# Kernel optimization log

Hardware: AMD Instinct MI355X
Metric: run time of the kernel (lower is better)

The kernel has to match this reference:

```python
import jax, jax.numpy as jnp
import numpy as np

DIM = 1536; FFN = 8960; NH = 12; HD = DIM // NH
B = 1; Fg, Hg, Wg = 8, 20, 20; L = Fg * Hg * Wg; L2 = 512
EPS = 1e-6; MAXLEN = 1024


def _rope_tables():
    # Wan rope_params: per-axis inverse-frequency tables, concatenated [t|h|w]
    c = HD // 2; c0 = c - 2 * (c // 3); c1 = c // 3
    def ang(dp):
        inv = 1.0 / (10000.0 ** (np.arange(0, dp, 2, dtype=np.float64) / dp))
        return np.outer(np.arange(MAXLEN, dtype=np.float64), inv)
    a = np.concatenate([ang(2 * c0), ang(2 * c1), ang(2 * c1)], axis=1)  # [1024, c]
    return np.cos(a).astype(np.float32), np.sin(a).astype(np.float32)


def setup_inputs() -> dict:
    key = jax.random.key(0)
    ks = jax.random.split(key, 32); it = iter(range(32))
    def rnd(shape, scale=0.02):
        return jax.random.normal(ks[next(it)], shape, dtype=jnp.float32) * scale
    cos, sin = _rope_tables()
    inp = {
        'x': rnd((B, L, DIM), 1.0),
        'e': rnd((B, 6, DIM), 1.0),
        'context': rnd((B, L2, DIM), 1.0),
        'freqs_cos': jnp.asarray(cos), 'freqs_sin': jnp.asarray(sin),
        'modulation': rnd((1, 6, DIM), DIM ** -0.5),
    }
    for p in ['sa', 'ca']:
        for nm in ['q', 'k', 'v', 'o']:
            inp[p + '_' + nm + 'w'] = rnd((DIM, DIM))
            inp[p + '_' + nm + 'b'] = jnp.zeros((DIM,), jnp.float32)
        inp[p + '_nq'] = jnp.ones((DIM,), jnp.float32)
        inp[p + '_nk'] = jnp.ones((DIM,), jnp.float32)
    inp['n3_w'] = jnp.ones((DIM,), jnp.float32); inp['n3_b'] = jnp.zeros((DIM,), jnp.float32)
    inp['ffn_w1'] = rnd((DIM, FFN)); inp['ffn_b1'] = jnp.zeros((FFN,), jnp.float32)
    inp['ffn_w2'] = rnd((FFN, DIM)); inp['ffn_b2'] = jnp.zeros((DIM,), jnp.float32)
    inp['grid_f'] = Fg; inp['grid_h'] = Hg; inp['grid_w'] = Wg
    return inp


def _layer_norm(x, w=None, b=None):
    mu = x.mean(-1, keepdims=True)
    var = jnp.mean((x - mu) ** 2, -1, keepdims=True)
    y = (x - mu) * jax.lax.rsqrt(var + EPS)
    return y * w + b if w is not None else y


def _rms(x, w):
    return x * jax.lax.rsqrt(jnp.mean(x * x, -1, keepdims=True) + EPS) * w


def _rope(xq, cos, sin, f, h, w):
    # xq: [B, L, n, d]; complex rotation per (t,h,w) axis with split freq dims
    b, s, n, d = xq.shape
    c = d // 2; c0 = c - 2 * (c // 3); c1 = c // 3
    def grid(tab):
        t = jnp.broadcast_to(tab[:f, None, None, :c0], (f, h, w, c0))
        hh = jnp.broadcast_to(tab[None, :h, None, c0:c0 + c1], (f, h, w, c1))
        ww = jnp.broadcast_to(tab[None, None, :w, c0 + c1:c0 + 2 * c1], (f, h, w, c1))
        return jnp.concatenate([t, hh, ww], -1).reshape(f * h * w, c)
    gc = grid(cos)[None, :, None, :]  # [1, L, 1, c]
    gs = grid(sin)[None, :, None, :]
    xr = xq.reshape(b, s, n, c, 2)
    xre, xim = xr[..., 0], xr[..., 1]
    return jnp.stack([xre * gc - xim * gs, xre * gs + xim * gc], -1).reshape(b, s, n, d)


def _attn(q, k, v):
    scores = jnp.einsum('bqnd,bknd->bnqk', q, k) * (q.shape[-1] ** -0.5)
    p = jax.nn.softmax(scores, -1)
    return jnp.einsum('bnqk,bknd->bqnd', p, v)


def reference(x, e, context, freqs_cos, freqs_sin, modulation,
              sa_qw, sa_qb, sa_kw, sa_kb, sa_vw, sa_vb, sa_ow, sa_ob, sa_nq, sa_nk,
              ca_qw, ca_qb, ca_kw, ca_kb, ca_vw, ca_vb, ca_ow, ca_ob, ca_nq, ca_nk,
              n3_w, n3_b, ffn_w1, ffn_b1, ffn_w2, ffn_b2,
              grid_f, grid_h, grid_w):
    b, s, _ = x.shape; n, d = NH, HD
    em = modulation + e  # [B, 6, C]
    e0, e1, e2, e3, e4, e5 = (em[:, i:i + 1] for i in range(6))
    # self-attention with adaLN modulation
    xs = _layer_norm(x) * (1 + e1) + e0
    q = _rms(xs @ sa_qw + sa_qb, sa_nq).reshape(b, s, n, d)
    k = _rms(xs @ sa_kw + sa_kb, sa_nk).reshape(b, s, n, d)
    v = (xs @ sa_vw + sa_vb).reshape(b, s, n, d)
    q = _rope(q, freqs_cos, freqs_sin, grid_f, grid_h, grid_w)
    k = _rope(k, freqs_cos, freqs_sin, grid_f, grid_h, grid_w)
    y = _attn(q, k, v).reshape(b, s, -1) @ sa_ow + sa_ob
    x = x + y * e2
    # cross-attention on norm3(x)
    xc = _layer_norm(x, n3_w, n3_b)
    s2 = context.shape[1]
    cq = _rms(xc @ ca_qw + ca_qb, ca_nq).reshape(b, s, n, d)
    ck = _rms(context @ ca_kw + ca_kb, ca_nk).reshape(b, s2, n, d)
    cv = (context @ ca_vw + ca_vb).reshape(b, s2, n, d)
    x = x + (_attn(cq, ck, cv).reshape(b, s, -1) @ ca_ow + ca_ob)
    # FFN with adaLN modulation
    xf = _layer_norm(x) * (1 + e4) + e3
    y = jax.nn.gelu(xf @ ffn_w1 + ffn_b1, approximate=True) @ ffn_w2 + ffn_b2
    return x + y * e5
```

## Files before the change

kernel.cpp:

```cpp
#include <hip/hip_runtime.h>

#define DIM 1536
#define NH 12
#define HD 128
#define LQ 3200
#define LKV 512
#define FFN 8960

typedef __attribute__((ext_vector_type(8))) short bf16x8;
typedef __attribute__((ext_vector_type(4))) float f32x4;
typedef __attribute__((ext_vector_type(4))) unsigned short u16x4;

__device__ inline unsigned short f2b(float f){
  union { float f; unsigned u; } x; x.f = f;
  unsigned r = (x.u + 0x7FFFu + ((x.u >> 16) & 1u)) >> 16;
  return (unsigned short)r;
}
__device__ inline float b2f(unsigned short u){
  union { unsigned u; float f; } x; x.u = ((unsigned)u) << 16; return x.f;
}
__device__ inline unsigned pack2(float a, float b){
  return (unsigned)f2b(a) | ((unsigned)f2b(b) << 16);
}
__device__ inline f32x4 mfma16(bf16x8 a, bf16x8 b, f32x4 c){
  return __builtin_amdgcn_mfma_f32_16x16x32_bf16(a, b, c, 0, 0, 0);
}
__device__ inline void gload_lds16(const unsigned short* g, unsigned short* l){
  __builtin_amdgcn_global_load_lds((const __attribute__((address_space(1))) unsigned int*)g,
                                   (__attribute__((address_space(3))) unsigned int*)l, 16, 0, 0);
}
__device__ inline int xcd_swizzle(int orig, int nwg){
  int q = nwg >> 3, r = nwg & 7;
  int xcd = orig & 7, off = orig >> 3;
  return (xcd < r ? xcd*(q+1) : r*(q+1) + (xcd-r)*q) + off;
}
__device__ inline float gelu_f(float vv){
  float u = 0.79788456080286535588f*(vv + 0.044715f*vv*vv*vv);
  u = fminf(fmaxf(u, -20.f), 20.f);
  float e2u = __expf(2.f*u);
  float th = (e2u - 1.f)/(e2u + 1.f);
  return 0.5f*vv*(1.f+th);
}


__global__ void add_vec(const float* __restrict__ a, const float* __restrict__ b,
                        float* __restrict__ o, int n){
  int i = blockIdx.x*256 + threadIdx.x;
  if (i < n) o[i] = a[i] + b[i];
}

__global__ void convert_bf16(const float* __restrict__ a, unsigned short* __restrict__ o, int n){
  int i = blockIdx.x*256 + threadIdx.x;
  if (i < n) o[i] = f2b(a[i]);
}

__global__ void concat3(const float* __restrict__ a, const float* __restrict__ b,
                        const float* __restrict__ c, float* __restrict__ o, int n){
  int i = blockIdx.x*256 + threadIdx.x;
  if (i < n) o[i] = a[i];
  else if (i < 2*n) o[i] = b[i - n];
  else if (i < 3*n) o[i] = c[i - 2*n];
}

__global__ void transpose_conv(const float* __restrict__ src, unsigned short* __restrict__ dst,
                               int K, int N){
  __shared__ float tile[32][33];
  int n0 = blockIdx.x*32, k0 = blockIdx.y*32;
  int tx = threadIdx.x, ty = threadIdx.y;
  #pragma unroll
  for (int i = 0; i < 4; i++)
    tile[ty + 8*i][tx] = src[(size_t)(k0 + ty + 8*i)*N + n0 + tx];
  __syncthreads();
  #pragma unroll
  for (int i = 0; i < 4; i++)
    dst[(size_t)(n0 + ty + 8*i)*K + k0 + tx] = f2b(tile[tx][ty + 8*i]);
}

__global__ __launch_bounds__(256) void ln_mod_kernel(const float* __restrict__ x,
    const float* __restrict__ mulv, const float* __restrict__ addv, int one_plus,
    unsigned short* __restrict__ out){
  int row = blockIdx.x;
  const float* xr = x + (size_t)row * DIM;
  int tid = threadIdx.x;
  float v[6]; float s = 0.f, ss = 0.f;
  #pragma unroll
  for (int i = 0; i < 6; i++){ v[i] = xr[tid + i*256]; s += v[i]; ss += v[i]*v[i]; }
  #pragma unroll
  for (int m = 1; m < 64; m <<= 1){ s += __shfl_xor(s, m, 64); ss += __shfl_xor(ss, m, 64); }
  __shared__ float bs[4], bss[4];
  int w = tid >> 6;
  if ((tid & 63) == 0){ bs[w] = s; bss[w] = ss; }
  __syncthreads();
  s = bs[0]+bs[1]+bs[2]+bs[3]; ss = bss[0]+bss[1]+bss[2]+bss[3];
  float mu  = s * (1.f/DIM);
  float var = ss * (1.f/DIM) - mu*mu;
  float inv = rsqrtf(var + 1e-6f);
  unsigned short* orow = out + (size_t)row*DIM;
  #pragma unroll
  for (int i = 0; i < 6; i++){
    int c = tid + i*256;
    float g = one_plus ? (1.f + mulv[c]) : mulv[c];
    orow[c] = f2b((v[i]-mu)*inv*g + addv[c]);
  }
}

__global__ __launch_bounds__(256) void reduce_ln_kernel(const float* P0, const float* P1,
    const float* bias, const float* resid, const float* svec, float* out_x,
    const float* mulv, const float* addv, int one_plus, unsigned short* out_ln){
  int row = blockIdx.x;
  size_t base = (size_t)row * DIM;
  int tid = threadIdx.x;
  float v[6]; float s = 0.f, ss = 0.f;
  #pragma unroll
  for (int i = 0; i < 6; i++){
    int c = tid + i*256;
    float sv = svec ? svec[c] : 1.f;
    float y = resid[base + c] + (P0[base + c] + P1[base + c] + bias[c])*sv;
    out_x[base + c] = y;
    v[i] = y; s += y; ss += y*y;
  }
  #pragma unroll
  for (int m = 1; m < 64; m <<= 1){ s += __shfl_xor(s, m, 64); ss += __shfl_xor(ss, m, 64); }
  __shared__ float bs[4], bss[4];
  int w = tid >> 6;
  if ((tid & 63) == 0){ bs[w] = s; bss[w] = ss; }
  __syncthreads();
  s = bs[0]+bs[1]+bs[2]+bs[3]; ss = bss[0]+bss[1]+bss[2]+bss[3];
  float mu  = s * (1.f/DIM);
  float var = ss * (1.f/DIM) - mu*mu;
  float inv = rsqrtf(var + 1e-6f);
  unsigned short* orow = out_ln + base;
  #pragma unroll
  for (int i = 0; i < 6; i++){
    int c = tid + i*256;
    float g = one_plus ? (1.f + mulv[c]) : mulv[c];
    orow[c] = f2b((v[i]-mu)*inv*g + addv[c]);
  }
}

__global__ __launch_bounds__(256) void reduce_rms_kernel(const float* __restrict__ P0,
    const float* __restrict__ P1, const float* __restrict__ bias,
    const float* __restrict__ nw, unsigned short* __restrict__ out){
  int row = blockIdx.x;
  size_t base = (size_t)row * DIM;
  int tid = threadIdx.x;
  float v[6]; float ss = 0.f;
  #pragma unroll
  for (int i = 0; i < 6; i++){
    int c = tid + i*256;
    float y = P0[base + c] + P1[base + c] + bias[c];
    v[i] = y; ss += y*y;
  }
  #pragma unroll
  for (int m = 1; m < 64; m <<= 1) ss += __shfl_xor(ss, m, 64);
  __shared__ float bss[4];
  if ((tid & 63) == 0) bss[tid >> 6] = ss;
  __syncthreads();
  ss = bss[0]+bss[1]+bss[2]+bss[3];
  float inv = rsqrtf(ss*(1.f/DIM) + 1e-6f);
  #pragma unroll
  for (int i = 0; i < 6; i++){
    int c = tid + i*256;
    out[base + c] = f2b(v[i]*inv*nw[c]);
  }
}

__global__ __launch_bounds__(256) void rms_rope_qk(unsigned short* __restrict__ buf,
    const float* __restrict__ nwq, const float* __restrict__ nwk,
    const float* __restrict__ ct, const float* __restrict__ st){
  int row = blockIdx.x;
  int sl = blockIdx.y;
  const float* nw = sl ? nwk : nwq;
  unsigned short* xr = buf + (size_t)row*(3*DIM) + sl*DIM;
  int tid = threadIdx.x;
  float ss = 0.f; float v[6];
  #pragma unroll
  for (int i = 0; i < 6; i++){ v[i] = b2f(xr[tid + i*256]); ss += v[i]*v[i]; }
  #pragma unroll
  for (int m = 1; m < 64; m <<= 1) ss += __shfl_xor(ss, m, 64);
  __shared__ float bss[4];
  if ((tid & 63) == 0) bss[tid >> 6] = ss;
  __syncthreads();
  ss = bss[0]+bss[1]+bss[2]+bss[3];
  float inv = rsqrtf(ss*(1.f/DIM) + 1e-6f);
  int f = row/400, hp = (row/20)%20, wp = row%20;
  for (int p = tid; p < 768; p += 256){
    int hh = p >> 6, j = p & 63;
    int pos = (j < 22) ? f : ((j < 43) ? hp : wp);
    float c_ = ct[pos*64 + j], s_ = st[pos*64 + j];
    int base = hh*HD + 2*j;
    float xre = b2f(xr[base])   * inv * nw[base];
    float xim = b2f(xr[base+1]) * inv * nw[base+1];
    xr[base]   = f2b(xre*c_ - xim*s_);
    xr[base+1] = f2b(xre*s_ + xim*c_);
  }
}

__global__ __launch_bounds__(256) void rms_rope_b16(unsigned short* __restrict__ buf, int ld,
    const float* __restrict__ nw){
  int row = blockIdx.x;
  unsigned short* xr = buf + (size_t)row*ld;
  int tid = threadIdx.x;
  float ss = 0.f; float v[6];
  #pragma unroll
  for (int i = 0; i < 6; i++){ v[i] = b2f(xr[tid + i*256]); ss += v[i]*v[i]; }
  #pragma unroll
  for (int m = 1; m < 64; m <<= 1) ss += __shfl_xor(ss, m, 64);
  __shared__ float bss[4];
  if ((tid & 63) == 0) bss[tid >> 6] = ss;
  __syncthreads();
  ss = bss[0]+bss[1]+bss[2]+bss[3];
  float inv = rsqrtf(ss*(1.f/DIM) + 1e-6f);
  #pragma unroll
  for (int i = 0; i < 6; i++){ int c = tid + i*256; xr[c] = f2b(v[i]*inv*nw[c]); }
}

__global__ __launch_bounds__(256) void packvt_kernel(const unsigned short* __restrict__ pre, int ld,
    unsigned short* __restrict__ VT, int ntok){
  int h = blockIdx.y; int t0 = blockIdx.x*64;
  __shared__ unsigned short tile[128][72];
  int tid = threadIdx.x;
  int d = tid & 127, tl = tid >> 7;
  #pragma unroll 4
  for (int i = 0; i < 32; i++){
    int tok = t0 + tl + 2*i;
    tile[d][tl + 2*i] = pre[(size_t)tok*ld + h*HD + d];
  }
  __syncthreads();
  int dd = tid >> 6, tl2 = tid & 63;
  #pragma unroll 4
  for (int i = 0; i < 32; i++){
    int d2 = dd + 4*i;
    VT[((size_t)h*HD + d2)*ntok + t0 + tl2] = tile[d2][tl2];
  }
}

__global__ void reduce_f32(const float* P0, const float* P1,
    const float* bias, const float* resid,
    const float* svec, float* out, int total4){
  int i = blockIdx.x*256 + threadIdx.x;
  if (i >= total4) return;
  int col = (i*4) % DIM;
  float4 p0 = ((const float4*)P0)[i];
  float4 p1 = ((const float4*)P1)[i];
  float4 rs = ((const float4*)resid)[i];
  float4 o;
  float s0 = svec ? svec[col]   : 1.f;
  float s1 = svec ? svec[col+1] : 1.f;
  float s2 = svec ? svec[col+2] : 1.f;
  float s3 = svec ? svec[col+3] : 1.f;
  o.x = rs.x + (p0.x + p1.x + bias[col])*s0;
  o.y = rs.y + (p0.y + p1.y + bias[col+1])*s1;
  o.z = rs.z + (p0.z + p1.z + bias[col+2])*s2;
  o.w = rs.w + (p0.w + p1.w + bias[col+3])*s3;
  ((float4*)out)[i] = o;
}

__global__ __launch_bounds__(512, 4) void gemm128_kernel(const unsigned short* __restrict__ A,
    const unsigned short* __restrict__ WT, const float* __restrict__ bias,
    int M, int N, int ldA, int ksize, int ep,
    float* __restrict__ outf0, float* __restrict__ outf1, unsigned short* __restrict__ outb){
  __shared__ unsigned short As[2][128*32];
  __shared__ unsigned short Bs[2][128*32];
  int t = threadIdx.x;
  int wv = t >> 6, lane = t & 63;
  int lr = lane & 15, lk = lane >> 4;
  int gx = gridDim.x;
  int nwg = gx * gridDim.y;
  int wg = xcd_swizzle(blockIdx.y*gx + blockIdx.x, nwg);
  int m0 = (wg % gx)*128, n0 = (wg / gx)*128;
  int kbeg = blockIdx.z*ksize;
  int wm = (wv >> 1)*32, wn = (wv & 1)*64;
  f32x4 z = {0.f,0.f,0.f,0.f};
  f32x4 acc[2][4];
  #pragma unroll
  for (int i = 0; i < 2; i++)
    #pragma unroll
    for (int j = 0; j < 4; j++) acc[i][j] = z;

  int srow = t >> 2;
  int sslot = (t & 3) ^ (srow & 3);
  const unsigned short* Ap0 = A  + (size_t)(m0 + srow)*ldA + kbeg + sslot*8;
  const unsigned short* Bp0 = WT + (size_t)(n0 + srow)*ldA + kbeg + sslot*8;
  int slA = (lk ^ (lr & 3))*8;

  int nk = ksize >> 5;
  gload_lds16(Ap0, &As[0][wv*512]);
  gload_lds16(Bp0, &Bs[0][wv*512]);
  asm volatile("s_waitcnt vmcnt(0)" ::: "memory");
  __syncthreads();

  for (int tt = 0; tt < nk; ++tt){
    int cur = tt & 1;
    if (tt + 1 < nk){
      int kn = (tt + 1) << 5;
      gload_lds16(Ap0 + kn, &As[cur^1][wv*512]);
      gload_lds16(Bp0 + kn, &Bs[cur^1][wv*512]);
    }
    bf16x8 af[2], bfr[4];
    #pragma unroll
    for (int i = 0; i < 2; i++)
      af[i]  = *(const bf16x8*)&As[cur][(wm + i*16 + lr)*32 + slA];
    #pragma unroll
    for (int j = 0; j < 4; j++)
      bfr[j] = *(const bf16x8*)&Bs[cur][(wn + j*16 + lr)*32 + slA];
    #pragma unroll
    for (int i = 0; i < 2; i++)
      #pragma unroll
      for (int j = 0; j < 4; j++)
        acc[i][j] = mfma16(af[i], bfr[j], acc[i][j]);
    asm volatile("s_waitcnt vmcnt(0)" ::: "memory");
    __syncthreads();
  }

  float* pdst = blockIdx.z ? outf1 : outf0;
  #pragma unroll
  for (int i = 0; i < 2; i++)
    #pragma unroll
    for (int j = 0; j < 4; j++)
      #pragma unroll
      for (int r = 0; r < 4; r++){
        int row = m0 + wm + i*16 + lk*4 + r;
        int col = n0 + wn + j*16 + lr;
        size_t idx = (size_t)row*N + col;
        if (ep == 4){
          pdst[idx] = acc[i][j][r];
        } else if (ep == 3){
          outb[idx] = f2b(acc[i][j][r] + bias[col]);
        } else {
          outb[idx] = f2b(gelu_f(acc[i][j][r] + bias[col]));
        }
      }
}

__global__ __launch_bounds__(512, 4) void gemmw_kernel(const unsigned short* __restrict__ A,
    const unsigned short* __restrict__ WT, const float* __restrict__ bias,
    int M, int N, int ldA, int K, int ep, unsigned short* __restrict__ outb){
  __shared__ unsigned short As[2][128*32];
  __shared__ unsigned short Bs[2][256*32];
  int t = threadIdx.x;
  int wv = t >> 6, lane = t & 63;
  int lr = lane & 15, lk = lane >> 4;
  int gx = gridDim.x;
  int wg = xcd_swizzle(blockIdx.y*gx + blockIdx.x, gx*gridDim.y);
  int m0 = (wg % gx)*128, n0 = (wg / gx)*256;
  int wm = (wv >> 2)*64, wn = (wv & 3)*64;
  f32x4 z = {0.f,0.f,0.f,0.f};
  f32x4 acc[4][4];
  #pragma unroll
  for (int i = 0; i < 4; i++)
    #pragma unroll
    for (int j = 0; j < 4; j++) acc[i][j] = z;

  int srow = t >> 2;
  int sslot = (t & 3) ^ (srow & 3);
  const unsigned short* Ap0 = A  + (size_t)(m0 + srow)*ldA + sslot*8;
  const unsigned short* Bp0 = WT + (size_t)(n0 + srow)*ldA + sslot*8;
  const unsigned short* Bp1 = WT + (size_t)(n0 + 128 + srow)*ldA + sslot*8;
  int slA = (lk ^ (lr & 3))*8;

  int nk = K >> 5;
  gload_lds16(Ap0, &As[0][wv*512]);
  gload_lds16(Bp0, &Bs[0][wv*512]);
  gload_lds16(Bp1, &Bs[0][4096 + wv*512]);
  asm volatile("s_waitcnt vmcnt(0)" ::: "memory");
  __syncthreads();

  for (int tt = 0; tt < nk; ++tt){
    int cur = tt & 1;
    if (tt + 1 < nk){
      int kn = (tt + 1) << 5;
      gload_lds16(Ap0 + kn, &As[cur^1][wv*512]);
      gload_lds16(Bp0 + kn, &Bs[cur^1][wv*512]);
      gload_lds16(Bp1 + kn, &Bs[cur^1][4096 + wv*512]);
    }
    bf16x8 af[4], bfr[4];
    #pragma unroll
    for (int i = 0; i < 4; i++)
      af[i]  = *(const bf16x8*)&As[cur][(wm + i*16 + lr)*32 + slA];
    #pragma unroll
    for (int j = 0; j < 4; j++)
      bfr[j] = *(const bf16x8*)&Bs[cur][(wn + j*16 + lr)*32 + slA];
    #pragma unroll
    for (int i = 0; i < 4; i++)
      #pragma unroll
      for (int j = 0; j < 4; j++)
        acc[i][j] = mfma16(af[i], bfr[j], acc[i][j]);
    asm volatile("s_waitcnt vmcnt(0)" ::: "memory");
    __syncthreads();
  }

  #pragma unroll
  for (int i = 0; i < 4; i++)
    #pragma unroll
    for (int j = 0; j < 4; j++)
      #pragma unroll
      for (int r = 0; r < 4; r++){
        int row = m0 + wm + i*16 + lk*4 + r;
        int col = n0 + wn + j*16 + lr;
        size_t idx = (size_t)row*N + col;
        float vv = acc[i][j][r] + bias[col];
        outb[idx] = (ep == 3) ? f2b(vv) : f2b(gelu_f(vv));
      }
}

__global__ __launch_bounds__(256, 3) void attn_kernel(const unsigned short* __restrict__ Q, int ldQ,
    const unsigned short* __restrict__ Kg, int ldK, const unsigned short* __restrict__ VT,
    unsigned short* __restrict__ O, int nkv, int vlen){
  __shared__ unsigned short Kls[64*128];
  __shared__ unsigned short Vls[128*64];
  __shared__ unsigned short Pls[4][16][80];
  int gx = gridDim.x;
  int wg = xcd_swizzle(blockIdx.y*gx + blockIdx.x, gx*gridDim.y);
  int bq = wg % gx, h = wg / gx;
  int tid = threadIdx.x;
  int wv = tid >> 6, lane = tid & 63;
  int lr = lane & 15, lk = lane >> 4;
  int q0 = bq*64 + wv*16;

  bf16x8 qf[4];
  const unsigned short* qp = Q + (size_t)(q0 + lr)*ldQ + h*HD + lk*8;
  #pragma unroll
  for (int kk = 0; kk < 4; kk++) qf[kk] = *(const bf16x8*)(qp + kk*32);

  f32x4 z = {0.f,0.f,0.f,0.f};
  f32x4 acc[8];
  #pragma unroll
  for (int d = 0; d < 8; d++) acc[d] = z;
  float mrun = -1e30f, lrun = 0.f;
  const float sc = 0.08838834764831845f;
  int swz = (lr & 7) << 4;

  for (int kt = 0; kt < nkv; kt += 64){
    __syncthreads();
    #pragma unroll
    for (int j = 0; j < 4; j++){
      int row = wv*16 + j*4 + (lane >> 4);
      int cb  = ((lane & 15)*16) ^ ((row & 7) << 4);
      gload_lds16(Kg + (size_t)(kt + row)*ldK + h*HD + (cb >> 1),
                  &Kls[(wv*16 + j*4)*128]);
    }
    #pragma unroll
    for (int j = 0; j < 4; j++){
      int d  = wv*32 + j*8 + (lane >> 3);
      int cb = ((lane & 7)*16) ^ ((d & 7) << 4);
      gload_lds16(VT + ((size_t)h*HD + d)*vlen + kt + (cb >> 1),
                  &Vls[(wv*32 + j*8)*64]);
    }
    asm volatile("s_waitcnt vmcnt(0)" ::: "memory");
    __syncthreads();

    f32x4 s[4];
    #pragma unroll
    for (int t4 = 0; t4 < 4; t4++) s[t4] = z;
    #pragma unroll
    for (int t4 = 0; t4 < 4; t4++){
      #pragma unroll
      for (int kk = 0; kk < 4; kk++){
        bf16x8 kf = *(const bf16x8*)&Kls[(t4*16 + lr)*128 + (((kk*64 + lk*16) ^ swz) >> 1)];
        s[t4] = mfma16(kf, qf[kk], s[t4]);
      }
    }

    float vv[4][4]; float pmax = -1e30f;
    #pragma unroll
    for (int t4 = 0; t4 < 4; t4++)
      #pragma unroll
      for (int r = 0; r < 4; r++){
        float xv = s[t4][r]*sc; vv[t4][r] = xv; pmax = fmaxf(pmax, xv);
      }
    pmax = fmaxf(pmax, __shfl_xor(pmax, 16, 64));
    pmax = fmaxf(pmax, __shfl_xor(pmax, 32, 64));

    if (__all(pmax - mrun <= 8.f)){
      float rs = 0.f;
      #pragma unroll
      for (int t4 = 0; t4 < 4; t4++)
        #pragma unroll
        for (int r = 0; r < 4; r++){
          float pv = __expf(vv[t4][r] - mrun); vv[t4][r] = pv; rs += pv;
        }
      rs += __shfl_xor(rs, 16, 64);
      rs += __shfl_xor(rs, 32, 64);
      lrun += rs;
    } else {
      float mn = fmaxf(mrun, pmax);
      float cr = __expf(mrun - mn);
      mrun = mn;
      float rs = 0.f;
      #pragma unroll
      for (int t4 = 0; t4 < 4; t4++)
        #pragma unroll
        for (int r = 0; r < 4; r++){
          float pv = __expf(vv[t4][r] - mn); vv[t4][r] = pv; rs += pv;
        }
      rs += __shfl_xor(rs, 16, 64);
      rs += __shfl_xor(rs, 32, 64);
      lrun = lrun*cr + rs;
      #pragma unroll
      for (int d = 0; d < 8; d++) acc[d] *= cr;
    }

    #pragma unroll
    for (int t4 = 0; t4 < 4; t4++){
      *(unsigned*)&Pls[wv][lr][t4*16 + lk*4]     = pack2(vv[t4][0], vv[t4][1]);
      *(unsigned*)&Pls[wv][lr][t4*16 + lk*4 + 2] = pack2(vv[t4][2], vv[t4][3]);
    }
    bf16x8 pb0 = *(const bf16x8*)&Pls[wv][lr][lk*8];
    bf16x8 pb1 = *(const bf16x8*)&Pls[wv][lr][32 + lk*8];

    #pragma unroll
    for (int db = 0; db < 8; db++){
      bf16x8 vf0 = *(const bf16x8*)&Vls[(db*16 + lr)*64 + (((lk*16) ^ swz) >> 1)];
      acc[db] = mfma16(vf0, pb0, acc[db]);
      bf16x8 vf1 = *(const bf16x8*)&Vls[(db*16 + lr)*64 + (((64 + lk*16) ^ swz) >> 1)];
      acc[db] = mfma16(vf1, pb1, acc[db]);
    }
  }

  float inv = 1.f/lrun;
  unsigned short* op = O + (size_t)(q0 + lr)*DIM + h*HD + lk*4;
  #pragma unroll
  for (int db = 0; db < 8; db++){
    u16x4 ov;
    ov[0] = f2b(acc[db][0]*inv); ov[1] = f2b(acc[db][1]*inv);
    ov[2] = f2b(acc[db][2]*inv); ov[3] = f2b(acc[db][3]*inv);
    *(u16x4*)(op + db*16) = ov;
  }
}


extern "C" void kernel_launch(void* const* d_in, const int* in_sizes, int n_in,
                              void* d_out, int out_size, void* d_ws, size_t ws_size,
                              hipStream_t stream){
  const float* x    = (const float*)d_in[0];
  const float* e    = (const float*)d_in[1];
  const float* ctx  = (const float*)d_in[2];
  const float* fcos = (const float*)d_in[3];
  const float* fsin = (const float*)d_in[4];
  const float* modu = (const float*)d_in[5];
  const float* sa_qw = (const float*)d_in[6];  const float* sa_qb = (const float*)d_in[7];
  const float* sa_kw = (const float*)d_in[8];  const float* sa_kb = (const float*)d_in[9];
  const float* sa_vw = (const float*)d_in[10]; const float* sa_vb = (const float*)d_in[11];
  const float* sa_ow = (const float*)d_in[12]; const float* sa_ob = (const float*)d_in[13];
  const float* sa_nq = (const float*)d_in[14]; const float* sa_nk = (const float*)d_in[15];
  const float* ca_qw = (const float*)d_in[16]; const float* ca_qb = (const float*)d_in[17];
  const float* ca_kw = (const float*)d_in[18]; const float* ca_kb = (const float*)d_in[19];
  const float* ca_vw = (const float*)d_in[20]; const float* ca_vb = (const float*)d_in[21];
  const float* ca_ow = (const float*)d_in[22]; const float* ca_ob = (const float*)d_in[23];
  const float* ca_nq = (const float*)d_in[24]; const float* ca_nk = (const float*)d_in[25];
  const float* n3w = (const float*)d_in[26]; const float* n3b = (const float*)d_in[27];
  const float* fw1 = (const float*)d_in[28]; const float* fb1 = (const float*)d_in[29];
  const float* fw2 = (const float*)d_in[30]; const float* fb2 = (const float*)d_in[31];

  char* p = (char*)d_ws;
  auto alloc = [&](size_t bytes){ void* r = (void*)p; p += (bytes + 255) & ~(size_t)255; return r; };
  unsigned short* wt[8];
  for (int i = 0; i < 8; i++) wt[i] = (unsigned short*)alloc((size_t)DIM*DIM*2);
  unsigned short* wtf1 = (unsigned short*)alloc((size_t)FFN*DIM*2);
  unsigned short* wtf2 = (unsigned short*)alloc((size_t)DIM*FFN*2);
  float* em     = (float*)alloc(6*DIM*4);
  float* qkvb   = (float*)alloc(3*DIM*4);
  float* ckvb   = (float*)alloc(2*DIM*4);
  unsigned short* nbuf = (unsigned short*)alloc((size_t)LQ*DIM*2);
  unsigned short* qkv16 = (unsigned short*)alloc((size_t)LQ*3*DIM*2);
  unsigned short* VTb   = (unsigned short*)alloc((size_t)LQ*DIM*2);
  unsigned short* Qb    = (unsigned short*)alloc((size_t)LQ*DIM*2);
  unsigned short* Ob    = (unsigned short*)alloc((size_t)LQ*DIM*2);
  float* x1 = (float*)alloc((size_t)LQ*DIM*4);
  unsigned short* ctxb   = (unsigned short*)alloc((size_t)LKV*DIM*2);
  unsigned short* cakv16 = (unsigned short*)alloc((size_t)LKV*2*DIM*2);

  float* P0   = (float*)d_out;
  float* P1a  = (float*)qkv16;
  float* P1f  = (float*)wtf1;
  unsigned short* hbuf = qkv16;
  const int TOT4 = LQ*DIM/4;

  add_vec<<<36, 256, 0, stream>>>(modu, e, em, 6*DIM);
  concat3<<<18, 256, 0, stream>>>(sa_qb, sa_kb, sa_vb, qkvb, DIM);
  concat3<<<12, 256, 0, stream>>>(ca_kb, ca_vb, ca_vb, ckvb, DIM);
  const float* wsrc[8] = {sa_qw, sa_kw, sa_vw, sa_ow, ca_qw, ca_kw, ca_vw, ca_ow};
  for (int i = 0; i < 8; i++)
    transpose_conv<<<dim3(48,48), dim3(32,8), 0, stream>>>(wsrc[i], wt[i], DIM, DIM);
  transpose_conv<<<dim3(280,48), dim3(32,8), 0, stream>>>(fw1, wtf1, DIM, FFN);
  transpose_conv<<<dim3(48,280), dim3(32,8), 0, stream>>>(fw2, wtf2, FFN, DIM);
  convert_bf16<<<(LKV*DIM)/256, 256, 0, stream>>>(ctx, ctxb, LKV*DIM);

  ln_mod_kernel<<<LQ, 256, 0, stream>>>(x, em + DIM, em, 1, nbuf);
  gemmw_kernel<<<dim3(25,18), 512, 0, stream>>>(nbuf, wt[0], qkvb, LQ, 3*DIM, DIM, DIM, 3, qkv16);
  rms_rope_qk<<<dim3(LQ,2), 256, 0, stream>>>(qkv16, sa_nq, sa_nk, fcos, fsin);
  packvt_kernel<<<dim3(50,12), 256, 0, stream>>>(qkv16 + 2*DIM, 3*DIM, VTb, LQ);
  attn_kernel<<<dim3(50,12), 256, 0, stream>>>(qkv16, 3*DIM, qkv16 + DIM, 3*DIM, VTb, Ob, LQ, LQ);
  gemm128_kernel<<<dim3(25,12,2), 512, 0, stream>>>(Ob, wt[3], nullptr, LQ, DIM, DIM, DIM/2, 4,
                                                    P0, P1a, nullptr);
  reduce_ln_kernel<<<LQ, 256, 0, stream>>>(P0, P1a, sa_ob, x, em + 2*DIM, x1,
                                           n3w, n3b, 0, nbuf);

  gemm128_kernel<<<dim3(25,12,2), 512, 0, stream>>>(nbuf, wt[4], nullptr, LQ, DIM, DIM, DIM/2, 4,
                                                    P0, P1a, nullptr);
  reduce_rms_kernel<<<LQ, 256, 0, stream>>>(P0, P1a, ca_qb, ca_nq, Qb);
  gemm128_kernel<<<dim3(4,24,1), 512, 0, stream>>>(ctxb, wt[5], ckvb, LKV, 2*DIM, DIM, DIM, 3,
                                                   nullptr, nullptr, cakv16);
  rms_rope_b16<<<LKV, 256, 0, stream>>>(cakv16, 2*DIM, ca_nk);
  packvt_kernel<<<dim3(8,12), 256, 0, stream>>>(cakv16 + DIM, 2*DIM, VTb, LKV);
  attn_kernel<<<dim3(50,12), 256, 0, stream>>>(Qb, DIM, cakv16, 2*DIM, VTb, Ob, LKV, LKV);
  gemm128_kernel<<<dim3(25,12,2), 512, 0, stream>>>(Ob, wt[7], nullptr, LQ, DIM, DIM, DIM/2, 4,
                                                    P0, P1a, nullptr);
  reduce_ln_kernel<<<LQ, 256, 0, stream>>>(P0, P1a, ca_ob, x1, nullptr, x1,
                                           em + 4*DIM, em + 3*DIM, 1, nbuf);

  gemmw_kernel<<<dim3(25,35), 512, 0, stream>>>(nbuf, wtf1, fb1, LQ, FFN, DIM, DIM, 2, hbuf);
  gemm128_kernel<<<dim3(25,12,2), 512, 0, stream>>>(hbuf, wtf2, nullptr, LQ, DIM, FFN, FFN/2, 4,
                                                    P0, P1f, nullptr);
  reduce_f32<<<(TOT4+255)/256, 256, 0, stream>>>(P0, P1f, fb2, x1, em + 5*DIM, (float*)d_out, TOT4);
}
```

Measured before the change: 777.5 us.

## Split self-attention over two KV halves and merge with a combine kernel

Self-attention now launches two blocks per (query tile, head), each processing half of the key/value sequence and writing a partial bf16 output plus its running max and sum. A new combine kernel rescales and sums the two partials per head into the final output. This doubles the grid from 600 to 1200 blocks to fill the GPU's CUs better. The cost is an extra kernel launch, an extra round trip of partial outputs through memory, and partials rounded to bf16 before combining. Two scratch buffers (Qb, x1) are reused for the partials.

After: 758.1 us, median of 3. 1.03x faster.

```diff
diff --git a/kernel.cpp b/kernel.cpp
--- a/kernel.cpp
+++ b/kernel.cpp
@@ -406,13 +406,16 @@
 
 __global__ __launch_bounds__(256, 3) void attn_kernel(const unsigned short* __restrict__ Q, int ldQ,
     const unsigned short* __restrict__ Kg, int ldK, const unsigned short* __restrict__ VT,
-    unsigned short* __restrict__ O, int nkv, int vlen){
+    unsigned short* O, int nkv, int vlen, int kvchunk,
+    float2* ml, unsigned short* op0, unsigned short* op1){
   __shared__ unsigned short Kls[64*128];
   __shared__ unsigned short Vls[128*64];
   __shared__ unsigned short Pls[4][16][80];
   int gx = gridDim.x;
   int wg = xcd_swizzle(blockIdx.y*gx + blockIdx.x, gx*gridDim.y);
   int bq = wg % gx, h = wg / gx;
+  int zi = blockIdx.z;
+  int kv0 = zi*kvchunk;
   int tid = threadIdx.x;
   int wv = tid >> 6, lane = tid & 63;
   int lr = lane & 15, lk = lane >> 4;
@@ -431,7 +434,7 @@
   const float sc = 0.08838834764831845f;
   int swz = (lr & 7) << 4;
 
-  for (int kt = 0; kt < nkv; kt += 64){
+  for (int kt = kv0; kt < kv0 + kvchunk; kt += 64){
     __syncthreads();
     #pragma unroll
     for (int j = 0; j < 4; j++){
@@ -519,13 +522,49 @@
   }
 
   float inv = 1.f/lrun;
-  unsigned short* op = O + (size_t)(q0 + lr)*DIM + h*HD + lk*4;
+  unsigned short* od = (gridDim.z == 1) ? O : (zi ? op1 : op0);
+  unsigned short* op = od + (size_t)(q0 + lr)*DIM + h*HD + lk*4;
   #pragma unroll
   for (int db = 0; db < 8; db++){
     u16x4 ov;
     ov[0] = f2b(acc[db][0]*inv); ov[1] = f2b(acc[db][1]*inv);
     ov[2] = f2b(acc[db][2]*inv); ov[3] = f2b(acc[db][3]*inv);
     *(u16x4*)(op + db*16) = ov;
+  }
+  if (gridDim.z > 1 && lk == 0)
+    ml[((size_t)zi*NH + h)*LQ + (q0 + lr)] = make_float2(mrun, lrun);
+}
+
+__global__ __launch_bounds__(256) void attn_combine(const unsigned short* __restrict__ op0,
+    const unsigned short* __restrict__ op1, const float2* __restrict__ ml,
+    unsigned short* __restrict__ O){
+  int row = blockIdx.x;
+  int tid = threadIdx.x;
+  __shared__ float w0s[NH], w1s[NH];
+  if (tid < NH){
+    float2 a = ml[(size_t)tid*LQ + row];
+    float2 b = ml[((size_t)NH + tid)*LQ + row];
+    float ms = fmaxf(a.x, b.x);
+    float e0 = __expf(a.x - ms)*a.y;
+    float e1 = __expf(b.x - ms)*b.y;
+    float inv = 1.f/(e0 + e1);
+    w0s[tid] = e0*inv; w1s[tid] = e1*inv;
+  }
+  __syncthreads();
+  size_t base = (size_t)row*DIM;
+  #pragma unroll
+  for (int i = 0; i < 2; i++){
+    int c4 = tid + i*256;
+    if (c4 < 384){
+      int h = c4 >> 5;
+      u16x4 a = *(const u16x4*)(op0 + base + c4*4);
+      u16x4 b = *(const u16x4*)(op1 + base + c4*4);
+      u16x4 o;
+      #pragma unroll
+      for (int j = 0; j < 4; j++)
+        o[j] = f2b(b2f(a[j])*w0s[h] + b2f(b[j])*w1s[h]);
+      *(u16x4*)(O + base + c4*4) = o;
+    }
   }
 }
 
@@ -562,6 +601,7 @@
   float* em     = (float*)alloc(6*DIM*4);
   float* qkvb   = (float*)alloc(3*DIM*4);
   float* ckvb   = (float*)alloc(2*DIM*4);
+  float2* mlb   = (float2*)alloc((size_t)2*NH*LQ*sizeof(float2));
   unsigned short* nbuf = (unsigned short*)alloc((size_t)LQ*DIM*2);
   unsigned short* qkv16 = (unsigned short*)alloc((size_t)LQ*3*DIM*2);
   unsigned short* VTb   = (unsigned short*)alloc((size_t)LQ*DIM*2);
@@ -575,6 +615,8 @@
   float* P1a  = (float*)qkv16;
   float* P1f  = (float*)wtf1;
   unsigned short* hbuf = qkv16;
+  unsigned short* opz0 = Qb;
+  unsigned short* opz1 = (unsigned short*)x1;
   const int TOT4 = LQ*DIM/4;
 
   add_vec<<<36, 256, 0, stream>>>(modu, e, em, 6*DIM);
@@ -591,7 +633,9 @@
   gemmw_kernel<<<dim3(25,18), 512, 0, stream>>>(nbuf, wt[0], qkvb, LQ, 3*DIM, DIM, DIM, 3, qkv16);
   rms_rope_qk<<<dim3(LQ,2), 256, 0, stream>>>(qkv16, sa_nq, sa_nk, fcos, fsin);
   packvt_kernel<<<dim3(50,12), 256, 0, stream>>>(qkv16 + 2*DIM, 3*DIM, VTb, LQ);
-  attn_kernel<<<dim3(50,12), 256, 0, stream>>>(qkv16, 3*DIM, qkv16 + DIM, 3*DIM, VTb, Ob, LQ, LQ);
+  attn_kernel<<<dim3(50,12,2), 256, 0, stream>>>(qkv16, 3*DIM, qkv16 + DIM, 3*DIM, VTb,
+                                                 nullptr, LQ, LQ, LQ/2, mlb, opz0, opz1);
+  attn_combine<<<LQ, 256, 0, stream>>>(opz0, opz1, mlb, Ob);
   gemm128_kernel<<<dim3(25,12,2), 512, 0, stream>>>(Ob, wt[3], nullptr, LQ, DIM, DIM, DIM/2, 4,
                                                     P0, P1a, nullptr);
   reduce_ln_kernel<<<LQ, 256, 0, stream>>>(P0, P1a, sa_ob, x, em + 2*DIM, x1,
@@ -604,7 +648,8 @@
                                                    nullptr, nullptr, cakv16);
   rms_rope_b16<<<LKV, 256, 0, stream>>>(cakv16, 2*DIM, ca_nk);
   packvt_kernel<<<dim3(8,12), 256, 0, stream>>>(cakv16 + DIM, 2*DIM, VTb, LKV);
-  attn_kernel<<<dim3(50,12), 256, 0, stream>>>(Qb, DIM, cakv16, 2*DIM, VTb, Ob, LKV, LKV);
+  attn_kernel<<<dim3(50,12,1), 256, 0, stream>>>(Qb, DIM, cakv16, 2*DIM, VTb,
+                                                 Ob, LKV, LKV, LKV, nullptr, nullptr, nullptr);
   gemm128_kernel<<<dim3(25,12,2), 512, 0, stream>>>(Ob, wt[7], nullptr, LQ, DIM, DIM, DIM/2, 4,
                                                     P0, P1a, nullptr);
   reduce_ln_kernel<<<LQ, 256, 0, stream>>>(P0, P1a, ca_ob, x1, nullptr, x1,
```
